# Kernel tuning notes

Hardware: AMD Instinct MI355X
Metric: run time of the kernel (lower is better)

Reference implementation:

```python
import jax, jax.numpy as jnp
import numpy as np

N, E = 50000, 400000
IN_DIM, TIME_DIM, OUT_DIM, H = 192, 64, 256, 4
D = OUT_DIM // H            # 64 per-head dim
GAT_IN = IN_DIM + TIME_DIM  # 256 == OUT_DIM -> identity residual path


def setup_inputs() -> dict:
    key = jax.random.key(0)
    ks = jax.random.split(key, 9)
    h = jax.random.normal(ks[0], (N, IN_DIM), jnp.float32)
    time_tensor = jax.random.uniform(ks[1], (E,), jnp.float32) * 100.0
    src = jax.random.randint(ks[2], (E,), 0, N, dtype=jnp.int32)
    dst = jax.random.randint(ks[3], (E,), 0, N, dtype=jnp.int32)
    time_w = jax.random.normal(ks[4], (TIME_DIM,), jnp.float32)
    time_b = jax.random.normal(ks[5], (TIME_DIM,), jnp.float32)
    fc_w = jax.random.normal(ks[6], (GAT_IN, H * D), jnp.float32) / np.float32(np.sqrt(GAT_IN))
    attn_l = jax.random.normal(ks[7], (H, D), jnp.float32) * 0.1
    attn_r = jax.random.normal(ks[8], (H, D), jnp.float32) * 0.1
    return {"h": h, "time_tensor": time_tensor, "src": src, "dst": dst,
            "time_w": time_w, "time_b": time_b, "fc_w": fc_w,
            "attn_l": attn_l, "attn_r": attn_r}


def reference(h, time_tensor, src, dst, time_w, time_b, fc_w, attn_l, attn_r):
    # --- temporal encoding per edge: cos(t * w + b) ---
    time_emb = jnp.cos(time_tensor[:, None] * time_w[None, :] + time_b[None, :])  # [E, T]
    # --- mean-aggregate incoming edge time features to nodes (fn.copy_e + fn.mean) ---
    deg = jax.ops.segment_sum(jnp.ones((E,), h.dtype), dst, num_segments=N)       # [N]
    agg_time = jax.ops.segment_sum(time_emb, dst, num_segments=N)
    agg_time = agg_time / jnp.maximum(deg, 1.0)[:, None]                          # [N, T]
    # --- concat node features with aggregated time features ---
    combined = jnp.concatenate([h, agg_time], axis=1)                             # [N, GAT_IN]
    # --- GAT projection and per-node attention logits ---
    feat = (combined @ fc_w).reshape(N, H, D)                                     # [N, H, D]
    el = jnp.einsum('nhd,hd->nh', feat, attn_l)                                   # [N, H]
    er = jnp.einsum('nhd,hd->nh', feat, attn_r)                                   # [N, H]
    # --- edge attention: u_add_v + leaky_relu ---
    e = jax.nn.leaky_relu(el[src] + er[dst], negative_slope=0.01)                 # [E, H]
    # --- edge_softmax over destination segments (numerically stable) ---
    emax = jax.lax.stop_gradient(jax.ops.segment_max(e, dst, num_segments=N))
    emax = jnp.where(jnp.isfinite(emax), emax, 0.0)
    ex = jnp.exp(e - emax[dst])
    denom = jax.ops.segment_sum(ex, dst, num_segments=N)
    a = ex / jnp.maximum(denom[dst], 1e-16)                                       # [E, H]
    # --- u_mul_e + sum aggregation ---
    msg = feat[src] * a[:, :, None]                                               # [E, H, D]
    rst = jax.ops.segment_sum(msg, dst, num_segments=N)                           # [N, H, D]
    # --- identity residual (in_feats == out_feats*num_heads) + elu ---
    rst = rst + combined.reshape(N, H, D)
    rst = jax.nn.elu(rst)
    return rst.reshape(N, OUT_DIM)
```

## Files before the change

kernel.cpp:

```cpp
#include <hip/hip_runtime.h>
#include <hip/hip_bf16.h>
#include <math.h>

#define N_NODES 50000
#define NP      50176
#define N_EDGES 400000
#define IN_DIM  192
#define NB      196

typedef float        f32x4 __attribute__((ext_vector_type(4)));
typedef unsigned int u32x4 __attribute__((ext_vector_type(4)));

__device__ __forceinline__ unsigned short f2bf(float f) {
    union { float f; unsigned int u; } v; v.f = f;
    unsigned int r = (v.u + 0x7FFF + ((v.u >> 16) & 1)) >> 16;
    return (unsigned short)r;
}
__device__ __forceinline__ float bfu_lo(unsigned int u) {
    union { unsigned int u; float f; } v; v.u = u << 16;
    return v.f;
}
__device__ __forceinline__ float bfu_hi(unsigned int u) {
    union { unsigned int u; float f; } v; v.u = u & 0xFFFF0000u;
    return v.f;
}

#define MFMA_BF16(acc, a, b) \
    asm("v_mfma_f32_16x16x32_bf16 %0, %1, %2, %0" : "+v"(acc) : "v"(a), "v"(b))

__global__ void k_hist(const int* __restrict__ dst, int* __restrict__ deg) {
    int e = blockIdx.x * 256 + threadIdx.x;
    if (e >= N_EDGES) return;
    atomicAdd(&deg[dst[e]], 1);
}

__global__ __launch_bounds__(256) void k_scanA(const int* __restrict__ deg,
                                               int* __restrict__ total,
                                               int* __restrict__ start,
                                               int* __restrict__ cursor) {
    __shared__ int part[256];
    __shared__ int base_s;
    int t = threadIdx.x;
    int i = blockIdx.x * 256 + t;
    int v = (i < N_NODES) ? deg[i] : 0;
    part[t] = v;
    __syncthreads();
#pragma unroll
    for (int off = 1; off < 256; off <<= 1) {
        int u = (t >= off) ? part[t - off] : 0;
        __syncthreads();
        part[t] += u;
        __syncthreads();
    }
    if (t == 255) base_s = atomicAdd(total, part[255]);
    __syncthreads();
    if (i < N_NODES) {
        int ex = base_s + part[t] - v;
        start[i] = ex;
        cursor[i] = ex;
    }
}

__global__ void k_bucket(const int* __restrict__ src, const int* __restrict__ dst,
                         const float* __restrict__ time_t, int* __restrict__ cursor,
                         int2* __restrict__ csr2) {
    int e = blockIdx.x * 256 + threadIdx.x;
    if (e >= N_EDGES) return;
    int d = dst[e];
    int idx = atomicAdd(&cursor[d], 1);
    csr2[idx] = make_int2(src[e], __float_as_int(time_t[e]));
}

__global__ void k_prep_w(const float* __restrict__ fw, unsigned short* __restrict__ wF) {
    int tid = blockIdx.x * 256 + threadIdx.x;
    int lane = tid & 63;
    int ks = (tid >> 6) & 7;
    int nt = tid >> 9;
    int c = lane & 15, g = lane >> 4;
    int n = nt * 16 + c;
    int k0 = ks * 32 + g * 8;
    union { unsigned short s[8]; u32x4 v; } u;
#pragma unroll
    for (int j = 0; j < 8; ++j) u.s[j] = f2bf(fw[(size_t)(k0 + j) * 256 + n]);
    *(u32x4*)(wF + (size_t)tid * 8) = u.v;
}

__global__ __launch_bounds__(256) void k_prep_a(const unsigned short* __restrict__ comb,
                                                unsigned short* __restrict__ aF) {
    int tid = blockIdx.x * 256 + threadIdx.x;
    int lane = tid & 63;
    int ks = (tid >> 6) & 7;
    int t = tid >> 9;
    int c = lane & 15, g = lane >> 4;
    u32x4 v = *(const u32x4*)(comb + (size_t)(t * 16 + c) * 256 + ks * 32 + g * 8);
    *(u32x4*)(aF + (size_t)tid * 8) = v;
}

__global__ void k_node_time(const float* __restrict__ h, const int2* __restrict__ csr2,
                            const int* __restrict__ start, const int* __restrict__ deg,
                            const float* __restrict__ tw, const float* __restrict__ tb,
                            unsigned short* __restrict__ comb) {
    int lane = threadIdx.x & 63;
    int wv   = threadIdx.x >> 6;
    int d = blockIdx.x * 4 + wv;
    if (d >= N_NODES) return;
    int k0 = start[d], dg = deg[d];
    float w = tw[lane], b = tb[lane];
    float s = 0.f;
    for (int kc = 0; kc < dg; kc += 64) {
        int cd = min(64, dg - kc);
        float tv = 0.f;
        if (lane < cd) tv = __int_as_float(csr2[k0 + kc + lane].y);
        for (int j = 0; j < cd; ++j) {
            float tj = __shfl(tv, j, 64);
            s += __cosf(tj * w + b);
        }
    }
    float mean = s / fmaxf((float)dg, 1.0f);
    const float* hr = h + (size_t)d * IN_DIM;
    unsigned short* orow = comb + (size_t)d * 256;
    orow[lane]       = f2bf(hr[lane]);
    orow[lane + 64]  = f2bf(hr[lane + 64]);
    orow[lane + 128] = f2bf(hr[lane + 128]);
    orow[lane + 192] = f2bf(mean);
}

__device__ __forceinline__ void gemm_epi(const f32x4 acc[16], int row_lo, int c,
                                         const float* __restrict__ al,
                                         const float* __restrict__ ar,
                                         unsigned short* __restrict__ feat,
                                         float* __restrict__ el,
                                         float* __restrict__ er) {
#pragma unroll
    for (int nt = 0; nt < 16; ++nt) {
#pragma unroll
        for (int reg = 0; reg < 4; ++reg) {
            feat[(size_t)(row_lo + reg) * 256 + nt * 16 + c] = f2bf(acc[nt][reg]);
        }
    }
#pragma unroll
    for (int hh = 0; hh < 4; ++hh) {
        float xl[4] = {0.f, 0.f, 0.f, 0.f};
        float xr[4] = {0.f, 0.f, 0.f, 0.f};
#pragma unroll
        for (int ntl = 0; ntl < 4; ++ntl) {
            int nt = hh * 4 + ntl;
            float av = al[nt * 16 + c];
            float rv = ar[nt * 16 + c];
#pragma unroll
            for (int reg = 0; reg < 4; ++reg) {
                xl[reg] += acc[nt][reg] * av;
                xr[reg] += acc[nt][reg] * rv;
            }
        }
#pragma unroll
        for (int reg = 0; reg < 4; ++reg) {
#pragma unroll
            for (int off = 1; off < 16; off <<= 1) {
                xl[reg] += __shfl_xor(xl[reg], off, 64);
                xr[reg] += __shfl_xor(xr[reg], off, 64);
            }
        }
        if (c == 0) {
#pragma unroll
            for (int reg = 0; reg < 4; ++reg) {
                el[(row_lo + reg) * 4 + hh] = xl[reg];
                er[(row_lo + reg) * 4 + hh] = xr[reg];
            }
        }
    }
}

__global__ __launch_bounds__(512) void k_gemm_mfma(
        const unsigned short* __restrict__ aF,
        const unsigned short* __restrict__ wF,
        const float* __restrict__ al, const float* __restrict__ ar,
        unsigned short* __restrict__ feat,
        float* __restrict__ el, float* __restrict__ er) {
    int lane = threadIdx.x & 63;
    int wave = threadIdx.x >> 6;
    int t0 = blockIdx.x * 8 + wave;
    int c = lane & 15;
    int g = lane >> 4;

    f32x4 acc[16];
#pragma unroll
    for (int nt = 0; nt < 16; ++nt) acc[nt] = (f32x4){0.f, 0.f, 0.f, 0.f};

    const unsigned short* ap = aF + ((size_t)(t0 * 8) * 64 + lane) * 8;
    const unsigned short* bp = wF + (size_t)lane * 8;

    for (int ks = 0; ks < 8; ++ks) {
        u32x4 a = *(const u32x4*)(ap + ks * 512);
#pragma unroll
        for (int nt = 0; nt < 16; ++nt) {
            u32x4 b = *(const u32x4*)(bp + (size_t)(nt * 8 + ks) * 512);
            MFMA_BF16(acc[nt], a, b);
        }
    }

    int row_lo = t0 * 16 + g * 4;
    gemm_epi(acc, row_lo, c, al, ar, feat, el, er);
}

#define CHUNK 64
__global__ __launch_bounds__(256) void k_node_agg(
        const int2* __restrict__ csr2,
        const int* __restrict__ start, const int* __restrict__ deg,
        const unsigned short* __restrict__ feat, const unsigned short* __restrict__ comb,
        const float* __restrict__ el, const float* __restrict__ er,
        float* __restrict__ out) {
    __shared__ float ex_lds[4][CHUNK * 4];
    __shared__ int   src_lds[4][CHUNK];
    int lane = threadIdx.x & 63;
    int wv   = threadIdx.x >> 6;
    int d = blockIdx.x * 4 + wv;
    int k0 = start[d], k1 = k0 + deg[d];
    int j4 = lane >> 2, h4 = lane & 3;
    int hh = lane >> 4;
    float er_a = er[d * 4 + h4];
    float acc0 = 0.f, acc1 = 0.f, acc2 = 0.f, acc3 = 0.f, den_part = 0.f;

    for (int kc = k0; kc < k1; kc += CHUNK) {
        int cd = min(CHUNK, k1 - kc);
        for (int p = 0; p * 16 < cd; ++p) {
            int j = p * 16 + j4;
            if (j < cd) {
                int s = csr2[kc + j].x;
                if (h4 == 0) src_lds[wv][j] = s;
                float v = el[s * 4 + h4] + er_a;
                v = v > 0.f ? v : 0.01f * v;
                float exv = __expf(v);
                ex_lds[wv][j * 4 + h4] = exv;
                den_part += exv;
            }
        }
#pragma unroll 2
        for (int j = 0; j < cd; ++j) {
            int s = src_lds[wv][j];
            float a = ex_lds[wv][j * 4 + hh];
            const uint2* fp = (const uint2*)(feat + (size_t)s * 256 + lane * 4);
            uint2 u = *fp;
            acc0 += bfu_lo(u.x) * a;
            acc1 += bfu_hi(u.x) * a;
            acc2 += bfu_lo(u.y) * a;
            acc3 += bfu_hi(u.y) * a;
        }
    }
    float dred = den_part;
    dred += __shfl_xor(dred, 4, 64);
    dred += __shfl_xor(dred, 8, 64);
    dred += __shfl_xor(dred, 16, 64);
    dred += __shfl_xor(dred, 32, 64);
    float den = __shfl(dred, hh, 64);
    float inv = 1.0f / fmaxf(den, 1e-16f);

    uint2 cb = *(const uint2*)(comb + (size_t)d * 256 + lane * 4);
    float x0 = bfu_lo(cb.x) + acc0 * inv;
    float x1 = bfu_hi(cb.x) + acc1 * inv;
    float x2 = bfu_lo(cb.y) + acc2 * inv;
    float x3 = bfu_hi(cb.y) + acc3 * inv;
    float4 o;
    o.x = x0 > 0.f ? x0 : expm1f(x0);
    o.y = x1 > 0.f ? x1 : expm1f(x1);
    o.z = x2 > 0.f ? x2 : expm1f(x2);
    o.w = x3 > 0.f ? x3 : expm1f(x3);
    *(float4*)&out[(size_t)d * 256 + lane * 4] = o;
}

extern "C" void kernel_launch(void* const* d_in, const int* in_sizes, int n_in,
                              void* d_out, int out_size, void* d_ws, size_t ws_size,
                              hipStream_t stream) {
    const float* h      = (const float*)d_in[0];
    const float* time_t = (const float*)d_in[1];
    const int*   src    = (const int*)d_in[2];
    const int*   dst    = (const int*)d_in[3];
    const float* tw     = (const float*)d_in[4];
    const float* tb     = (const float*)d_in[5];
    const float* fw     = (const float*)d_in[6];
    const float* al     = (const float*)d_in[7];
    const float* ar     = (const float*)d_in[8];
    float* out = (float*)d_out;

    char* p = (char*)d_ws;
    int*   deg      = (int*)p;                 p += 200000;
    int*   total    = (int*)p;                 p += 64;
    int*   start    = (int*)p;                 p += 200000;
    int*   cursor   = (int*)p;
    unsigned short* wF = (unsigned short*)p;   p += 200000;
    int2*  csr2     = (int2*)p;                p += 3200000;
    unsigned short* comb_bf = (unsigned short*)p; p += (size_t)NP * 512;
    unsigned short* feat_bf = (unsigned short*)p; p += (size_t)NP * 512;
    unsigned short* aF      = (unsigned short*)p; p += (size_t)NP * 512;
    float* el       = (float*)p;               p += (size_t)NP * 16;
    float* er       = (float*)p;               p += (size_t)NP * 16;

    hipMemsetAsync(d_ws, 0, 200064, stream);

    k_hist<<<(N_EDGES + 255) / 256, 256, 0, stream>>>(dst, deg);
    k_scanA<<<NB, 256, 0, stream>>>(deg, total, start, cursor);
    k_bucket<<<(N_EDGES + 255) / 256, 256, 0, stream>>>(src, dst, time_t, cursor, csr2);
    k_prep_w<<<32, 256, 0, stream>>>(fw, wF);
    k_node_time<<<N_NODES / 4, 256, 0, stream>>>(h, csr2, start, deg, tw, tb, comb_bf);
    k_prep_a<<<(NP / 16) * 2, 256, 0, stream>>>(comb_bf, aF);
    k_gemm_mfma<<<NP / 128, 512, 0, stream>>>(aF, wF, al, ar, feat_bf, el, er);
    k_node_agg<<<N_NODES / 4, 256, 0, stream>>>(csr2, start, deg, feat_bf, comb_bf, el, er, out);
}
```

Before: 159.5 us.

## Fuse time aggregation, A-fragment staging and MFMA GEMM into one kernel

Merges the per-node time-encoding kernel, the A-fragment repack kernel and the MFMA projection GEMM into a single kernel. Each wave computes 16 node rows into LDS, then feeds them directly to the MFMA loop, dropping the aF workspace buffer and two launches. It also gives cursor its own workspace region so the weight prep can run before bucketing. The cost is that each wave now serialises time aggregation over 16 nodes, leaving fewer waves to hide gather latency.

```diff
diff --git a/kernel.cpp b/kernel.cpp
--- a/kernel.cpp
+++ b/kernel.cpp
@@ -85,46 +85,6 @@
     *(u32x4*)(wF + (size_t)tid * 8) = u.v;
 }
 
-__global__ __launch_bounds__(256) void k_prep_a(const unsigned short* __restrict__ comb,
-                                                unsigned short* __restrict__ aF) {
-    int tid = blockIdx.x * 256 + threadIdx.x;
-    int lane = tid & 63;
-    int ks = (tid >> 6) & 7;
-    int t = tid >> 9;
-    int c = lane & 15, g = lane >> 4;
-    u32x4 v = *(const u32x4*)(comb + (size_t)(t * 16 + c) * 256 + ks * 32 + g * 8);
-    *(u32x4*)(aF + (size_t)tid * 8) = v;
-}
-
-__global__ void k_node_time(const float* __restrict__ h, const int2* __restrict__ csr2,
-                            const int* __restrict__ start, const int* __restrict__ deg,
-                            const float* __restrict__ tw, const float* __restrict__ tb,
-                            unsigned short* __restrict__ comb) {
-    int lane = threadIdx.x & 63;
-    int wv   = threadIdx.x >> 6;
-    int d = blockIdx.x * 4 + wv;
-    if (d >= N_NODES) return;
-    int k0 = start[d], dg = deg[d];
-    float w = tw[lane], b = tb[lane];
-    float s = 0.f;
-    for (int kc = 0; kc < dg; kc += 64) {
-        int cd = min(64, dg - kc);
-        float tv = 0.f;
-        if (lane < cd) tv = __int_as_float(csr2[k0 + kc + lane].y);
-        for (int j = 0; j < cd; ++j) {
-            float tj = __shfl(tv, j, 64);
-            s += __cosf(tj * w + b);
-        }
-    }
-    float mean = s / fmaxf((float)dg, 1.0f);
-    const float* hr = h + (size_t)d * IN_DIM;
-    unsigned short* orow = comb + (size_t)d * 256;
-    orow[lane]       = f2bf(hr[lane]);
-    orow[lane + 64]  = f2bf(hr[lane + 64]);
-    orow[lane + 128] = f2bf(hr[lane + 128]);
-    orow[lane + 192] = f2bf(mean);
-}
-
 __device__ __forceinline__ void gemm_epi(const f32x4 acc[16], int row_lo, int c,
                                          const float* __restrict__ al,
                                          const float* __restrict__ ar,
@@ -171,35 +131,69 @@
     }
 }
 
-__global__ __launch_bounds__(512) void k_gemm_mfma(
-        const unsigned short* __restrict__ aF,
+__global__ __launch_bounds__(256) void k_fuse(
+        const float* __restrict__ h, const int2* __restrict__ csr2,
+        const int* __restrict__ start, const int* __restrict__ deg,
+        const float* __restrict__ tw, const float* __restrict__ tb,
         const unsigned short* __restrict__ wF,
         const float* __restrict__ al, const float* __restrict__ ar,
-        unsigned short* __restrict__ feat,
+        unsigned short* __restrict__ comb, unsigned short* __restrict__ feat,
         float* __restrict__ el, float* __restrict__ er) {
-    int lane = threadIdx.x & 63;
-    int wave = threadIdx.x >> 6;
-    int t0 = blockIdx.x * 8 + wave;
-    int c = lane & 15;
-    int g = lane >> 4;
-
+    __shared__ unsigned short stage[4][16][264];
+    int t = threadIdx.x;
+    int lane = t & 63, wv = t >> 6;
+    int tile = blockIdx.x * 4 + wv;
+    float w = tw[lane], b = tb[lane];
+
+    for (int i = 0; i < 16; ++i) {
+        int d = tile * 16 + i;
+        unsigned short v0 = 0, v1 = 0, v2 = 0, v3 = 0;
+        if (d < N_NODES) {
+            int k0 = start[d], dg = deg[d];
+            float s = 0.f;
+            for (int kc = 0; kc < dg; kc += 64) {
+                int cd = min(64, dg - kc);
+                float tv = 0.f;
+                if (lane < cd) tv = __int_as_float(csr2[k0 + kc + lane].y);
+                for (int j = 0; j < cd; ++j) {
+                    float tj = __shfl(tv, j, 64);
+                    s += __cosf(tj * w + b);
+                }
+            }
+            float mean = s / fmaxf((float)dg, 1.0f);
+            const float* hr = h + (size_t)d * IN_DIM;
+            v0 = f2bf(hr[lane]);
+            v1 = f2bf(hr[lane + 64]);
+            v2 = f2bf(hr[lane + 128]);
+            v3 = f2bf(mean);
+            unsigned short* orow = comb + (size_t)d * 256;
+            orow[lane]       = v0;
+            orow[lane + 64]  = v1;
+            orow[lane + 128] = v2;
+            orow[lane + 192] = v3;
+        }
+        stage[wv][i][lane]       = v0;
+        stage[wv][i][lane + 64]  = v1;
+        stage[wv][i][lane + 128] = v2;
+        stage[wv][i][lane + 192] = v3;
+    }
+
+    int c = lane & 15, g = lane >> 4;
     f32x4 acc[16];
 #pragma unroll
     for (int nt = 0; nt < 16; ++nt) acc[nt] = (f32x4){0.f, 0.f, 0.f, 0.f};
 
-    const unsigned short* ap = aF + ((size_t)(t0 * 8) * 64 + lane) * 8;
     const unsigned short* bp = wF + (size_t)lane * 8;
-
     for (int ks = 0; ks < 8; ++ks) {
-        u32x4 a = *(const u32x4*)(ap + ks * 512);
+        u32x4 a = *(const u32x4*)(&stage[wv][c][ks * 32 + g * 8]);
 #pragma unroll
         for (int nt = 0; nt < 16; ++nt) {
-            u32x4 b = *(const u32x4*)(bp + (size_t)(nt * 8 + ks) * 512);
-            MFMA_BF16(acc[nt], a, b);
-        }
-    }
-
-    int row_lo = t0 * 16 + g * 4;
+            u32x4 bb = *(const u32x4*)(bp + (size_t)(nt * 8 + ks) * 512);
+            MFMA_BF16(acc[nt], a, bb);
+        }
+    }
+
+    int row_lo = tile * 16 + g * 4;
     gemm_epi(acc, row_lo, c, al, ar, feat, el, er);
 }
 
@@ -286,12 +280,11 @@
     int*   deg      = (int*)p;                 p += 200000;
     int*   total    = (int*)p;                 p += 64;
     int*   start    = (int*)p;                 p += 200000;
-    int*   cursor   = (int*)p;
-    unsigned short* wF = (unsigned short*)p;   p += 200000;
+    int*   cursor   = (int*)p;                 p += 200000;
+    unsigned short* wF = (unsigned short*)p;   p += 131072;
     int2*  csr2     = (int2*)p;                p += 3200000;
     unsigned short* comb_bf = (unsigned short*)p; p += (size_t)NP * 512;
     unsigned short* feat_bf = (unsigned short*)p; p += (size_t)NP * 512;
-    unsigned short* aF      = (unsigned short*)p; p += (size_t)NP * 512;
     float* el       = (float*)p;               p += (size_t)NP * 16;
     float* er       = (float*)p;               p += (size_t)NP * 16;
 
@@ -299,10 +292,9 @@
 
     k_hist<<<(N_EDGES + 255) / 256, 256, 0, stream>>>(dst, deg);
     k_scanA<<<NB, 256, 0, stream>>>(deg, total, start, cursor);
+    k_prep_w<<<32, 256, 0, stream>>>(fw, wF);
     k_bucket<<<(N_EDGES + 255) / 256, 256, 0, stream>>>(src, dst, time_t, cursor, csr2);
-    k_prep_w<<<32, 256, 0, stream>>>(fw, wF);
-    k_node_time<<<N_NODES / 4, 256, 0, stream>>>(h, csr2, start, deg, tw, tb, comb_bf);
-    k_prep_a<<<(NP / 16) * 2, 256, 0, stream>>>(comb_bf, aF);
-    k_gemm_mfma<<<NP / 128, 512, 0, stream>>>(aF, wF, al, ar, feat_bf, el, er);
+    k_fuse<<<NP / 64, 256, 0, stream>>>(h, csr2, start, deg, tw, tb, wF, al, ar,
+                                        comb_bf, feat_bf, el, er);
     k_node_agg<<<N_NODES / 4, 256, 0, stream>>>(csr2, start, deg, feat_bf, comb_bf, el, er, out);
 }
```

Result: slower. 184.9 us (+15.9%).
